# Performance work log

Measured on AMD Instinct MI355X. Metric: run time of the kernel, lower is better.

Reference implementation:

```python
import jax, jax.numpy as jnp
import numpy as np

B, N, D, S = 64, 1024, 8, 16
SPARSE_PROB = 0.1


def setup_inputs() -> dict:
    key = jax.random.key(0)
    k_x, k_m, k_ws, k_bd, k_wd, k_bs = jax.random.split(key, 6)
    x = jax.random.normal(k_x, (B, N, D, S), dtype=jnp.float32)
    # conexao='esparsa': (rand < 0.1).float() buffer, exactly like _criar_matriz_conexao
    matriz_conexao = (jax.random.uniform(k_m, (N, N)) < SPARSE_PROB).astype(jnp.float32)
    # Stacked per-neuron parameters of NeuronioDendritico
    w_syn = jax.random.normal(k_ws, (N, D, S), dtype=jnp.float32) * 0.1   # synapse weights
    b_dend = jax.random.normal(k_bd, (N, D), dtype=jnp.float32) * 0.1     # dendrite bias
    w_dend = jax.random.normal(k_wd, (N, D), dtype=jnp.float32) * 0.1     # dendrite->soma weights
    b_soma = jax.random.normal(k_bs, (N,), dtype=jnp.float32) * 0.1       # soma bias
    return {"x": x, "matriz_conexao": matriz_conexao, "w_syn": w_syn,
            "b_dend": b_dend, "w_dend": w_dend, "b_soma": b_soma}


def reference(x, matriz_conexao, w_syn, b_dend, w_dend, b_soma):
    # Connectivity mixing across neurons (conexao != 'densa'):
    # torch.einsum('bids,oi->bods', x, matriz_conexao)
    xm = jnp.einsum('bids,oi->bods', x, matriz_conexao)  # [B, N, D, S]
    # Fused batched version of the Python loop over n_neurons:
    # each dendrite: tanh(sum_s w*x + b)
    dend = jnp.tanh(jnp.einsum('bnds,nds->bnd', xm, w_syn) + b_dend[None])  # [B, N, D]
    # soma: weighted sum of dendritic outputs + bias -> sigmoid spike
    soma = jnp.einsum('bnd,nd->bn', dend, w_dend) + b_soma[None]            # [B, N]
    spikes = jax.nn.sigmoid(soma)
    return spikes
```

## Files before the change

### kernel.cpp

```cpp
#include <hip/hip_runtime.h>
#include <hip/hip_bf16.h>

#define BB 64
#define NN 1024
#define DD 8
#define SS 16
#define DS 128

typedef __attribute__((ext_vector_type(8))) short short8;
typedef __attribute__((ext_vector_type(4))) float floatx4;

typedef __attribute__((address_space(1))) const unsigned int glds_src;
typedef __attribute__((address_space(3))) unsigned int glds_dst;

static __device__ __forceinline__ unsigned short f2bf(float f) {
    unsigned int u = __float_as_uint(f);
    unsigned int r = (u + 0x7FFFu + ((u >> 16) & 1u)) >> 16;
    return (unsigned short)r;
}

__global__ void prepass(const float* __restrict__ x, unsigned short* __restrict__ xT,
                        const float* __restrict__ M, unsigned short* __restrict__ Mb) {
    __shared__ float tile[64 * 68];
    const int t = threadIdx.x;

    if (blockIdx.x < 1024) {
        int i = (blockIdx.x * 256 + t) * 4;
        float4 v = *(const float4*)(M + i);
        unsigned int p0 = (unsigned int)f2bf(v.x) | ((unsigned int)f2bf(v.y) << 16);
        unsigned int p1 = (unsigned int)f2bf(v.z) | ((unsigned int)f2bf(v.w) << 16);
        *(uint2*)(Mb + i) = make_uint2(p0, p1);
        return;
    }

    const int bid = blockIdx.x - 1024;
    const int i0 = (bid & 15) * 64;
    const int c0 = ((bid >> 4) & 1) * 64;
    const int b  = bid >> 5;
    const float* xb = x + (size_t)b * (NN * DS);

#pragma unroll
    for (int jj = 0; jj < 4; ++jj) {
        int il = (t >> 4) + jj * 16;
        int cl = (t & 15) * 4;
        float4 v = *(const float4*)(xb + (size_t)(i0 + il) * DS + c0 + cl);
        *(float4*)(tile + il * 68 + cl) = v;
    }
    __syncthreads();
    int cr  = t >> 2;
    int iq  = (t & 3) * 16;
    int rot = (t & 3) * 2;
    unsigned int p[8];
#pragma unroll
    for (int j = 0; j < 8; ++j) {
        int jp = (j + rot) & 7;
        unsigned short lo = f2bf(tile[(iq + 2 * jp + 0) * 68 + cr]);
        unsigned short hi = f2bf(tile[(iq + 2 * jp + 1) * 68 + cr]);
        p[jp] = (unsigned int)lo | ((unsigned int)hi << 16);
    }
    unsigned short* dst = xT + (size_t)b * (NN * DS) + (size_t)(c0 + cr) * NN + i0 + iq;
    *(uint4*)(dst + 0) = make_uint4(p[0], p[1], p[2], p[3]);
    *(uint4*)(dst + 8) = make_uint4(p[4], p[5], p[6], p[7]);
}

__global__ __launch_bounds__(512, 2) void gemm_fused(
    const unsigned short* __restrict__ Mb,
    const unsigned short* __restrict__ xT,
    const float* __restrict__ w_syn,
    const float* __restrict__ b_dend,
    const float* __restrict__ w_dend,
    const float* __restrict__ b_soma,
    float* __restrict__ out)
{
    __shared__ __align__(16) unsigned short As[3 * 256 * 64];
    __shared__ __align__(16) unsigned short Bs[3 * 128 * 64];
    __shared__ float ex[256 * 4];

    const int t      = threadIdx.x;
    const int b      = blockIdx.x;
    const int o_base = blockIdx.y * 256;

    const int lane = t & 63;
    const int w    = t >> 6;
    const int wm   = w >> 2;
    const int wn   = w & 3;
    const int lm   = lane & 15;
    const int kq   = lane >> 4;

    const char* AgB = (const char*)(Mb + (size_t)o_base * NN);
    const char* BgB = (const char*)(xT + (size_t)b * (NN * DS));

    const int r8 = lane >> 3, l8 = lane & 7;
    const int sg = (l8 ^ r8) * 16;
    int offA[4], ldsA[4], offB[2], ldsB[2];
#pragma unroll
    for (int j = 0; j < 4; ++j) {
        offA[j] = (w * 32 + j * 8 + r8) * (NN * 2) + sg;
        ldsA[j] = (w * 32 + j * 8) * 128;
    }
#pragma unroll
    for (int j = 0; j < 2; ++j) {
        offB[j] = (w * 16 + j * 8 + r8) * (NN * 2) + sg;
        ldsB[j] = (w * 16 + j * 8) * 128;
    }

#define STAGE_H0(TT, BUF) do { const int kb_ = (TT) * 128;                                            \
    __builtin_amdgcn_global_load_lds((glds_src*)(AgB + offA[0] + kb_),                                \
        (glds_dst*)((char*)As + (BUF) * 32768 + ldsA[0]), 16, 0, 0);                                  \
    __builtin_amdgcn_global_load_lds((glds_src*)(AgB + offA[1] + kb_),                                \
        (glds_dst*)((char*)As + (BUF) * 32768 + ldsA[1]), 16, 0, 0);                                  \
    __builtin_amdgcn_global_load_lds((glds_src*)(BgB + offB[0] + kb_),                                \
        (glds_dst*)((char*)Bs + (BUF) * 16384 + ldsB[0]), 16, 0, 0);                                  \
} while (0)

#define STAGE_H1(TT, BUF) do { const int kb_ = (TT) * 128;                                            \
    __builtin_amdgcn_global_load_lds((glds_src*)(AgB + offA[2] + kb_),                                \
        (glds_dst*)((char*)As + (BUF) * 32768 + ldsA[2]), 16, 0, 0);                                  \
    __builtin_amdgcn_global_load_lds((glds_src*)(AgB + offA[3] + kb_),                                \
        (glds_dst*)((char*)As + (BUF) * 32768 + ldsA[3]), 16, 0, 0);                                  \
    __builtin_amdgcn_global_load_lds((glds_src*)(BgB + offB[1] + kb_),                                \
        (glds_dst*)((char*)Bs + (BUF) * 16384 + ldsB[1]), 16, 0, 0);                                  \
} while (0)

#define NOSTAGE do {} while (0)
#define VM6  asm volatile("s_waitcnt vmcnt(6)" ::: "memory")
#define VM0  asm volatile("s_waitcnt vmcnt(0)" ::: "memory")
#define NOVM do {} while (0)

#define PHASE(KS, BUFC, STMT_STAGE, STMT_VM) do {                                                     \
    const unsigned short* Ab_ = As + (BUFC) * 16384;                                                  \
    const unsigned short* Bb_ = Bs + (BUFC) * 8192;                                                   \
    short8 af_[8], bf_[2];                                                                            \
    const int gg_ = (((KS) * 4 + kq) ^ (lm & 7)) * 8;                                                 \
    _Pragma("unroll")                                                                                 \
    for (int m_ = 0; m_ < 8; ++m_)                                                                    \
        af_[m_] = *(const short8*)(Ab_ + (wm * 128 + m_ * 16 + lm) * 64 + gg_);                       \
    _Pragma("unroll")                                                                                 \
    for (int n_ = 0; n_ < 2; ++n_)                                                                    \
        bf_[n_] = *(const short8*)(Bb_ + (wn * 32 + n_ * 16 + lm) * 64 + gg_);                        \
    STMT_STAGE;                                                                                       \
    STMT_VM;                                                                                          \
    __builtin_amdgcn_s_barrier();                                                                     \
    asm volatile("s_waitcnt lgkmcnt(0)" ::: "memory");                                                \
    __builtin_amdgcn_sched_barrier(0);                                                                \
    __builtin_amdgcn_s_setprio(1);                                                                    \
    _Pragma("unroll")                                                                                 \
    for (int m_ = 0; m_ < 8; ++m_)                                                                    \
        _Pragma("unroll")                                                                             \
        for (int n_ = 0; n_ < 2; ++n_)                                                                \
            acc[m_][n_] = __builtin_amdgcn_mfma_f32_16x16x32_bf16(af_[m_], bf_[n_], acc[m_][n_], 0, 0, 0); \
    __builtin_amdgcn_s_setprio(0);                                                                    \
    __builtin_amdgcn_s_barrier();                                                                     \
} while (0)

    floatx4 acc[8][2] = {};

    STAGE_H0(0, 0); STAGE_H1(0, 0);
    STAGE_H0(1, 1); STAGE_H1(1, 1);
    VM6;
    __builtin_amdgcn_s_barrier();

    for (int kt = 0; kt < 14; ++kt) {
        const int bufc = kt % 3;
        const int bufs = (kt + 2) % 3;
        PHASE(0, bufc, STAGE_H0(kt + 2, bufs), NOVM);
        PHASE(1, bufc, STAGE_H1(kt + 2, bufs), VM6);
    }
    PHASE(0, 2, NOSTAGE, NOVM);
    PHASE(1, 2, NOSTAGE, VM0);
    PHASE(0, 0, NOSTAGE, NOVM);
    PHASE(1, 0, NOSTAGE, NOVM);

#undef PHASE
#undef STAGE_H0
#undef STAGE_H1

    float keep[2][2];
#pragma unroll
    for (int m = 0; m < 8; ++m) {
#pragma unroll
        for (int rg = 0; rg < 4; ++rg) {
            const int o = o_base + wm * 128 + m * 16 + kq * 4 + rg;
#pragma unroll
            for (int n = 0; n < 2; ++n) {
                const int d = wn * 2 + n;
                float p = acc[m][n][rg] * w_syn[o * DS + d * SS + lm];
                p += __shfl_xor(p, 1);
                p += __shfl_xor(p, 2);
                p += __shfl_xor(p, 4);
                p += __shfl_xor(p, 8);
                if (lm == (m & 3) * 4 + rg) keep[m >> 2][n] = p;
            }
        }
    }
#pragma unroll
    for (int mh = 0; mh < 2; ++mh) {
        const int o_loc = wm * 128 + mh * 64 + (lm >> 2) * 16 + kq * 4 + (lm & 3);
        const int o     = o_base + o_loc;
        float part = 0.f;
#pragma unroll
        for (int n = 0; n < 2; ++n) {
            const int d = wn * 2 + n;
            float pre = keep[mh][n] + b_dend[o * DD + d];
            part += tanhf(pre) * w_dend[o * DD + d];
        }
        ex[o_loc * 4 + wn] = part;
    }
    __syncthreads();
    if (t < 256) {
        float soma = ex[t * 4] + ex[t * 4 + 1] + ex[t * 4 + 2] + ex[t * 4 + 3]
                   + b_soma[o_base + t];
        out[(size_t)b * NN + o_base + t] = 1.f / (1.f + __expf(-soma));
    }
}

extern "C" void kernel_launch(void* const* d_in, const int* in_sizes, int n_in,
                              void* d_out, int out_size, void* d_ws, size_t ws_size,
                              hipStream_t stream) {
    const float* x      = (const float*)d_in[0];
    const float* M      = (const float*)d_in[1];
    const float* w_syn  = (const float*)d_in[2];
    const float* b_dend = (const float*)d_in[3];
    const float* w_dend = (const float*)d_in[4];
    const float* b_soma = (const float*)d_in[5];
    float* out = (float*)d_out;

    unsigned short* xT = (unsigned short*)d_ws;
    unsigned short* Mb = xT + (size_t)BB * NN * DS;

    prepass   <<<dim3(1024 + 2048), 256, 0, stream>>>(x, xT, M, Mb);
    gemm_fused<<<dim3(BB, NN / 256), 512, 0, stream>>>(Mb, xT, w_syn, b_dend, w_dend, b_soma, out);
}
```

Before: 111.4 us.

## Restructure GEMM mainloop to one barrier pair per k-tile with full-unrolled staging

Replaces the two-phase-per-tile schedule, which interleaved half-tile global->LDS staging with LDS fragment loads and used four barriers per tile. Each k-tile now issues all six async loads at once, waits on vmcnt(12), takes two barriers, then runs both k-substeps of LDS reads and MFMAs. The main loop is fully unrolled. The goal is fewer barriers and simpler scheduling, at the cost of less fine-grained overlap between LDS reads and MFMAs and more code size.

New measurement: 115.3 us. +3.5%, slower.

```diff
diff --git a/kernel.cpp b/kernel.cpp
--- a/kernel.cpp
+++ b/kernel.cpp
@@ -104,76 +104,66 @@
         ldsB[j] = (w * 16 + j * 8) * 128;
     }
 
-#define STAGE_H0(TT, BUF) do { const int kb_ = (TT) * 128;                                            \
+#define STAGE(TT, BUF) do { const int kb_ = (TT) * 128;                                               \
     __builtin_amdgcn_global_load_lds((glds_src*)(AgB + offA[0] + kb_),                                \
         (glds_dst*)((char*)As + (BUF) * 32768 + ldsA[0]), 16, 0, 0);                                  \
     __builtin_amdgcn_global_load_lds((glds_src*)(AgB + offA[1] + kb_),                                \
         (glds_dst*)((char*)As + (BUF) * 32768 + ldsA[1]), 16, 0, 0);                                  \
-    __builtin_amdgcn_global_load_lds((glds_src*)(BgB + offB[0] + kb_),                                \
-        (glds_dst*)((char*)Bs + (BUF) * 16384 + ldsB[0]), 16, 0, 0);                                  \
-} while (0)
-
-#define STAGE_H1(TT, BUF) do { const int kb_ = (TT) * 128;                                            \
     __builtin_amdgcn_global_load_lds((glds_src*)(AgB + offA[2] + kb_),                                \
         (glds_dst*)((char*)As + (BUF) * 32768 + ldsA[2]), 16, 0, 0);                                  \
     __builtin_amdgcn_global_load_lds((glds_src*)(AgB + offA[3] + kb_),                                \
         (glds_dst*)((char*)As + (BUF) * 32768 + ldsA[3]), 16, 0, 0);                                  \
+    __builtin_amdgcn_global_load_lds((glds_src*)(BgB + offB[0] + kb_),                                \
+        (glds_dst*)((char*)Bs + (BUF) * 16384 + ldsB[0]), 16, 0, 0);                                  \
     __builtin_amdgcn_global_load_lds((glds_src*)(BgB + offB[1] + kb_),                                \
         (glds_dst*)((char*)Bs + (BUF) * 16384 + ldsB[1]), 16, 0, 0);                                  \
 } while (0)
 
-#define NOSTAGE do {} while (0)
-#define VM6  asm volatile("s_waitcnt vmcnt(6)" ::: "memory")
-#define VM0  asm volatile("s_waitcnt vmcnt(0)" ::: "memory")
-#define NOVM do {} while (0)
-
-#define PHASE(KS, BUFC, STMT_STAGE, STMT_VM) do {                                                     \
+#define COMPUTE(BUFC) do {                                                                            \
     const unsigned short* Ab_ = As + (BUFC) * 16384;                                                  \
     const unsigned short* Bb_ = Bs + (BUFC) * 8192;                                                   \
-    short8 af_[8], bf_[2];                                                                            \
-    const int gg_ = (((KS) * 4 + kq) ^ (lm & 7)) * 8;                                                 \
-    _Pragma("unroll")                                                                                 \
-    for (int m_ = 0; m_ < 8; ++m_)                                                                    \
-        af_[m_] = *(const short8*)(Ab_ + (wm * 128 + m_ * 16 + lm) * 64 + gg_);                       \
-    _Pragma("unroll")                                                                                 \
-    for (int n_ = 0; n_ < 2; ++n_)                                                                    \
-        bf_[n_] = *(const short8*)(Bb_ + (wn * 32 + n_ * 16 + lm) * 64 + gg_);                        \
-    STMT_STAGE;                                                                                       \
-    STMT_VM;                                                                                          \
-    __builtin_amdgcn_s_barrier();                                                                     \
-    asm volatile("s_waitcnt lgkmcnt(0)" ::: "memory");                                                \
-    __builtin_amdgcn_sched_barrier(0);                                                                \
     __builtin_amdgcn_s_setprio(1);                                                                    \
     _Pragma("unroll")                                                                                 \
-    for (int m_ = 0; m_ < 8; ++m_)                                                                    \
+    for (int ks_ = 0; ks_ < 2; ++ks_) {                                                               \
+        short8 af_[8], bf_[2];                                                                        \
+        const int gg_ = (((ks_ * 4 + kq) ^ (lm & 7)) * 8);                                            \
+        _Pragma("unroll")                                                                             \
+        for (int m_ = 0; m_ < 8; ++m_)                                                                \
+            af_[m_] = *(const short8*)(Ab_ + (wm * 128 + m_ * 16 + lm) * 64 + gg_);                   \
         _Pragma("unroll")                                                                             \
         for (int n_ = 0; n_ < 2; ++n_)                                                                \
-            acc[m_][n_] = __builtin_amdgcn_mfma_f32_16x16x32_bf16(af_[m_], bf_[n_], acc[m_][n_], 0, 0, 0); \
+            bf_[n_] = *(const short8*)(Bb_ + (wn * 32 + n_ * 16 + lm) * 64 + gg_);                    \
+        _Pragma("unroll")                                                                             \
+        for (int m_ = 0; m_ < 8; ++m_)                                                                \
+            _Pragma("unroll")                                                                         \
+            for (int n_ = 0; n_ < 2; ++n_)                                                            \
+                acc[m_][n_] = __builtin_amdgcn_mfma_f32_16x16x32_bf16(af_[m_], bf_[n_], acc[m_][n_], 0, 0, 0); \
+    }                                                                                                 \
     __builtin_amdgcn_s_setprio(0);                                                                    \
-    __builtin_amdgcn_s_barrier();                                                                     \
 } while (0)
 
     floatx4 acc[8][2] = {};
 
-    STAGE_H0(0, 0); STAGE_H1(0, 0);
-    STAGE_H0(1, 1); STAGE_H1(1, 1);
-    VM6;
+    STAGE(0, 0);
+    STAGE(1, 1);
+
+#pragma unroll
+    for (int kt = 0; kt < 14; ++kt) {
+        __builtin_amdgcn_s_barrier();
+        STAGE(kt + 2, (kt + 2) % 3);
+        asm volatile("s_waitcnt vmcnt(12)" ::: "memory");
+        __builtin_amdgcn_s_barrier();
+        COMPUTE(kt % 3);
+    }
+    asm volatile("s_waitcnt vmcnt(6)" ::: "memory");
     __builtin_amdgcn_s_barrier();
-
-    for (int kt = 0; kt < 14; ++kt) {
-        const int bufc = kt % 3;
-        const int bufs = (kt + 2) % 3;
-        PHASE(0, bufc, STAGE_H0(kt + 2, bufs), NOVM);
-        PHASE(1, bufc, STAGE_H1(kt + 2, bufs), VM6);
-    }
-    PHASE(0, 2, NOSTAGE, NOVM);
-    PHASE(1, 2, NOSTAGE, VM0);
-    PHASE(0, 0, NOSTAGE, NOVM);
-    PHASE(1, 0, NOSTAGE, NOVM);
-
-#undef PHASE
-#undef STAGE_H0
-#undef STAGE_H1
+    COMPUTE(2);
+    asm volatile("s_waitcnt vmcnt(0)" ::: "memory");
+    __builtin_amdgcn_s_barrier();
+    COMPUTE(0);
+
+#undef STAGE
+#undef COMPUTE
 
     float keep[2][2];
 #pragma unroll
```
